# Performance work log

Hardware: AMD Instinct MI355X
Metric: run time of the kernel (lower is better)

Reference implementation:

```python
import jax, jax.numpy as jnp
import numpy as np

N = 50000   # nodes
E = 400000  # edges per relation
R = 3       # relations
IN, HID, OUT, H = 256, 64, 64, 4
NEG_SLOPE = 0.2


def setup_inputs() -> dict:
    key = jax.random.key(0)
    ks = jax.random.split(key, 16)
    w = lambda k, shape, s: jax.random.normal(k, shape, jnp.float32) * s
    sW = 1.0 / np.sqrt(IN)  # ~xavier scale (all fan-ins are 256)
    return {
        "x":   w(ks[0], (N, IN), 1.0),
        "src": jax.random.randint(ks[1], (R, E), 0, N, jnp.int32),
        "dst": jax.random.randint(ks[2], (R, E), 0, N, jnp.int32),
        "W0":  w(ks[3], (R, IN, H * HID), sW),
        "al0": w(ks[4], (R, H, HID), 0.1),
        "ar0": w(ks[5], (R, H, HID), 0.1),
        "b0":  jnp.zeros((R, H * HID), jnp.float32),
        "W1":  w(ks[6], (R, H * HID, H * HID), sW),
        "al1": w(ks[7], (R, H, HID), 0.1),
        "ar1": w(ks[8], (R, H, HID), 0.1),
        "b1":  jnp.zeros((R, H * HID), jnp.float32),
        "W2":  w(ks[9], (R, H * HID, H * OUT), sW),
        "al2": w(ks[10], (R, H, OUT), 0.1),
        "ar2": w(ks[11], (R, H, OUT), 0.1),
        "b2":  jnp.zeros((R, H * OUT), jnp.float32),
    }


def gat_conv(h, src, dst, W, al, ar, b):
    """One DGL-style GATConv with elu activation. h: (N, F_in)."""
    heads, d = al.shape
    feat = (h @ W).reshape(-1, heads, d)               # (N, H, D)
    el = jnp.einsum('nhd,hd->nh', feat, al)            # (N, H)
    er = jnp.einsum('nhd,hd->nh', feat, ar)
    e = jax.nn.leaky_relu(el[src] + er[dst], NEG_SLOPE)  # (E, H)
    # segment softmax over incoming edges of each dst node
    emax = jax.ops.segment_max(e, dst, num_segments=N)
    ex = jnp.exp(e - emax[dst])
    denom = jax.ops.segment_sum(ex, dst, num_segments=N)
    alpha = ex / jnp.maximum(denom[dst], 1e-9)         # (E, H)
    msg = feat[src] * alpha[:, :, None]                # (E, H, D)
    out = jax.ops.segment_sum(msg, dst, num_segments=N)  # (N, H, D)
    out = out + b.reshape(heads, d)
    return jax.nn.elu(out)


def _rgat(x, src, dst, params):
    h = x
    for li, (W, al, ar, b) in enumerate(params):
        outs = [gat_conv(h, src[r], dst[r], W[r], al[r], ar[r], b[r]) for r in range(R)]
        o = sum(outs) / R                              # cross-relation mean, (N, H, D)
        h = o.mean(1) if li == 2 else o.reshape(N, -1)
    return h


def reference(x, src, dst, W0, al0, ar0, b0, W1, al1, ar1, b1, W2, al2, ar2, b2):
    params = [(W0, al0, ar0, b0), (W1, al1, ar1, b1), (W2, al2, ar2, b2)]
    return _rgat(x, src, dst, params)
```

## Files before the change

### kernel.cpp

```cpp
#include <hip/hip_runtime.h>
#include <hip/hip_bf16.h>

#define N_NODES 50000
#define N_EDGES 400000
#define N_REL   3
#define NEG_SLOPE 0.2f
#define RP_STRIDE 50016
#define SCAN_BLOCKS 49
#define M_TILES 391
#define MG_PER_XCD 49
#define M_PAD 50048

typedef __bf16 bf16x8 __attribute__((ext_vector_type(8)));
typedef float  f32x4  __attribute__((ext_vector_type(4)));

static __device__ __forceinline__ float bf2f(unsigned short u) {
  return __uint_as_float(((unsigned)u) << 16);
}
static __device__ __forceinline__ unsigned short f2bf(float f) {
  union { float f; unsigned u; } x; x.f = f;
  unsigned r = x.u + 0x7FFFu + ((x.u >> 16) & 1u);
  return (unsigned short)(r >> 16);
}
static __device__ __forceinline__ void gld16(const void* g, unsigned short* lds) {
  __builtin_amdgcn_global_load_lds(
      (const __attribute__((address_space(1))) unsigned int*)g,
      (__attribute__((address_space(3))) unsigned int*)lds, 16, 0, 0);
}


__global__ void count_kernel(const int* __restrict__ dst, int* __restrict__ cnt, int total) {
  int i = blockIdx.x * 256 + threadIdx.x;
  if (i < total) {
    int r = i / N_EDGES;
    atomicAdd(&cnt[r * N_NODES + dst[i]], 1);
  }
}

__global__ void block_reduce_kernel(const int* __restrict__ cnt, int* __restrict__ psum) {
  __shared__ int s[256];
  int r = blockIdx.x / SCAN_BLOCKS, b = blockIdx.x % SCAN_BLOCKS;
  int node = b * 1024 + threadIdx.x * 4;
  int sum = 0;
  if (node + 3 < N_NODES) {
    int4 v = *(const int4*)&cnt[r * N_NODES + node];
    sum = v.x + v.y + v.z + v.w;
  } else {
    for (int j = 0; j < 4; j++)
      if (node + j < N_NODES) sum += cnt[r * N_NODES + node + j];
  }
  s[threadIdx.x] = sum;
  __syncthreads();
  for (int o = 128; o > 0; o >>= 1) {
    if (threadIdx.x < o) s[threadIdx.x] += s[threadIdx.x + o];
    __syncthreads();
  }
  if (threadIdx.x == 0) psum[r * SCAN_BLOCKS + b] = s[0];
}

__global__ void psum_scan_kernel(int* __restrict__ psum, int* __restrict__ row_ptr) {
  int r = blockIdx.x, t = threadIdx.x;
  int v = (t < SCAN_BLOCKS) ? psum[r * SCAN_BLOCKS + t] : 0;
  int incl = v;
#pragma unroll
  for (int o = 1; o < 64; o <<= 1) {
    int u = __shfl_up(incl, o);
    if (t >= o) incl += u;
  }
  if (t < SCAN_BLOCKS) psum[r * SCAN_BLOCKS + t] = incl - v;
  if (t == SCAN_BLOCKS - 1) row_ptr[r * RP_STRIDE + N_NODES] = incl;
}

__global__ void scan_write_kernel(const int* __restrict__ cnt, const int* __restrict__ psum,
                                  int* __restrict__ row_ptr, int* __restrict__ cursor) {
  __shared__ int s[256];
  int r = blockIdx.x / SCAN_BLOCKS, b = blockIdx.x % SCAN_BLOCKS;
  int tid = threadIdx.x;
  int node = b * 1024 + tid * 4;
  int c[4] = {0, 0, 0, 0};
  if (node + 3 < N_NODES) {
    int4 v = *(const int4*)&cnt[r * N_NODES + node];
    c[0] = v.x; c[1] = v.y; c[2] = v.z; c[3] = v.w;
  } else {
    for (int j = 0; j < 4; j++)
      if (node + j < N_NODES) c[j] = cnt[r * N_NODES + node + j];
  }
  int tsum = c[0] + c[1] + c[2] + c[3];
  s[tid] = tsum;
  __syncthreads();
  for (int o = 1; o < 256; o <<= 1) {
    int v = (tid >= o) ? s[tid - o] : 0;
    __syncthreads();
    s[tid] += v;
    __syncthreads();
  }
  int run = s[tid] - tsum + psum[r * SCAN_BLOCKS + b];
  if (node + 3 < N_NODES) {
    int4 rp = make_int4(run, run + c[0], run + c[0] + c[1], run + c[0] + c[1] + c[2]);
    *(int4*)&row_ptr[r * RP_STRIDE + node] = rp;
    *(int4*)&cursor[r * N_NODES + node] = rp;
  } else {
    for (int j = 0; j < 4; j++) {
      if (node + j < N_NODES) {
        row_ptr[r * RP_STRIDE + node + j] = run;
        cursor[r * N_NODES + node + j] = run;
      }
      run += c[j];
    }
  }
}

__global__ void scatter_kernel(const int* __restrict__ src, const int* __restrict__ dst,
                               int* __restrict__ cursor, int* __restrict__ col, int total) {
  int i = blockIdx.x * 256 + threadIdx.x;
  if (i < total) {
    int r = i / N_EDGES;
    int d = dst[i];
    int pos = atomicAdd(&cursor[r * N_NODES + d], 1);
    col[r * N_EDGES + pos] = src[i];
  }
}


__global__ void xsplit_kernel(const float* __restrict__ x, unsigned short* __restrict__ xh) {
  int i = blockIdx.x * 256 + threadIdx.x;
  int row = i >> 6;
  float4 v = make_float4(0.f, 0.f, 0.f, 0.f);
  if (row < N_NODES) v = ((const float4*)x)[i];
  ushort4 h;
  h.x = f2bf(v.x); h.y = f2bf(v.y); h.z = f2bf(v.z); h.w = f2bf(v.w);
  ((ushort4*)xh)[i] = h;
}


__global__ void wsplit_kernel(const float* __restrict__ W0, const float* __restrict__ W1,
                              const float* __restrict__ W2,
                              unsigned short* __restrict__ Whi, unsigned short* __restrict__ Wlo) {
  __shared__ float tile[32][33];
  int mat = blockIdx.x >> 6;
  int t = blockIdx.x & 63;
  int k0 = (t >> 3) * 32, n0 = (t & 7) * 32;
  const float* W = (mat < 3 ? W0 : (mat < 6 ? W1 : W2)) + (size_t)(mat % 3) * 65536;
  int row = threadIdx.x >> 3;
  int c4 = threadIdx.x & 7;
  float4 v = *(const float4*)&W[(k0 + row) * 256 + n0 + c4 * 4];
  tile[c4 * 4 + 0][row] = v.x;
  tile[c4 * 4 + 1][row] = v.y;
  tile[c4 * 4 + 2][row] = v.z;
  tile[c4 * 4 + 3][row] = v.w;
  __syncthreads();
  int nl = threadIdx.x >> 3;
  int kq = threadIdx.x & 7;
  ushort4 h, l;
  float a0 = tile[nl][kq * 4 + 0], a1 = tile[nl][kq * 4 + 1];
  float a2 = tile[nl][kq * 4 + 2], a3 = tile[nl][kq * 4 + 3];
  h.x = f2bf(a0); l.x = f2bf(a0 - bf2f(h.x));
  h.y = f2bf(a1); l.y = f2bf(a1 - bf2f(h.y));
  h.z = f2bf(a2); l.z = f2bf(a2 - bf2f(h.z));
  h.w = f2bf(a3); l.w = f2bf(a3 - bf2f(h.w));
  size_t o = (size_t)mat * 65536 + (n0 + nl) * 256 + k0 + kq * 4;
  *(ushort4*)&Whi[o] = h;
  *(ushort4*)&Wlo[o] = l;
}


#define LDS_S 32
#define LDT  136
#define PLANE 4096
#define BUFSZ (3 * PLANE)

__global__ __launch_bounds__(256, 3) void gemm_mfma_kernel(
    const unsigned short* __restrict__ Ah,
    const unsigned short* __restrict__ Bhi, const unsigned short* __restrict__ Blo,
    const float* __restrict__ alf, const float* __restrict__ arf,
    unsigned short* __restrict__ Cb, float* __restrict__ el, float* __restrict__ er, int M) {
  __shared__ __align__(16) unsigned short lds[2 * BUFSZ];

  const int wid = blockIdx.x;
  const int xcd = wid & 7, local = wid >> 3;
  const int m_t = (local / 6) * 8 + xcd;
  if (m_t >= M_TILES) return;
  const int n_t = local % 6;
  const int m0 = m_t * 128, n0 = n_t * 128;

  const int tid = threadIdx.x;
  const int wave = tid >> 6, lane = tid & 63;
  const int quad = lane >> 4, l16 = lane & 15;
  const int wr = wave & 1, wc = wave >> 1;

  f32x4 acc[4][4];
#pragma unroll
  for (int i = 0; i < 4; i++)
#pragma unroll
    for (int j = 0; j < 4; j++) acc[i][j] = (f32x4){0.f, 0.f, 0.f, 0.f};

  auto stage = [&](int kb, int b) {
    unsigned short* As = lds + b * BUFSZ;
#pragma unroll
    for (int i = 0; i < 2; i++) {
      int ch = wave * 2 + i;
      int c = ch * 64 + lane;
      int row = c >> 2, k16 = c & 3;
      int k16s = k16 ^ ((row >> 1) & 3);
      size_t gA = ((size_t)(m0 + row) * 256 + kb * 32) * 2 + (size_t)k16s * 16;
      size_t gB = ((size_t)(n0 + row) * 256 + kb * 32) * 2 + (size_t)k16s * 16;
      gld16((const char*)Ah + gA, &As[ch * 512]);
      gld16((const char*)Bhi + gB, &As[PLANE + ch * 512]);
      gld16((const char*)Blo + gB, &As[2 * PLANE + ch * 512]);
    }
  };

  stage(0, 0);
  __syncthreads();
  for (int kb = 0; kb < 8; kb++) {
    const int b = kb & 1;
    if (kb < 7) stage(kb + 1, b ^ 1);

    const unsigned short* As = lds + b * BUFSZ;
    const unsigned short* Bh = As + PLANE;
    const unsigned short* Bl = As + 2 * PLANE;
    bf16x8 ah[4], bh[4], bl[4];
#pragma unroll
    for (int t = 0; t < 4; t++) {
      int ar = wr * 64 + t * 16 + l16;
      int br = wc * 64 + t * 16 + l16;
      int ac = quad ^ ((ar >> 1) & 3);
      int bc = quad ^ ((br >> 1) & 3);
      ah[t] = *(const bf16x8*)&As[ar * LDS_S + ac * 8];
      bh[t] = *(const bf16x8*)&Bh[br * LDS_S + bc * 8];
      bl[t] = *(const bf16x8*)&Bl[br * LDS_S + bc * 8];
    }
#pragma unroll
    for (int mi = 0; mi < 4; mi++)
#pragma unroll
      for (int ni = 0; ni < 4; ni++) {
        acc[mi][ni] = __builtin_amdgcn_mfma_f32_16x16x32_bf16(ah[mi], bl[ni], acc[mi][ni], 0, 0, 0);
        acc[mi][ni] = __builtin_amdgcn_mfma_f32_16x16x32_bf16(ah[mi], bh[ni], acc[mi][ni], 0, 0, 0);
      }
    __syncthreads();
  }

  const int hw = n_t * 2 + wc;
  const int rel = hw >> 2, hh = hw & 3;
  float alw[4], arw[4];
#pragma unroll
  for (int ni = 0; ni < 4; ni++) {
    int gc = n0 + wc * 64 + ni * 16 + l16;
    alw[ni] = alf[gc]; arw[ni] = arf[gc];
  }
  float pel[4][4], per_[4][4];
#pragma unroll
  for (int mi = 0; mi < 4; mi++)
#pragma unroll
    for (int r = 0; r < 4; r++) {
      float se = 0.f, sr = 0.f;
#pragma unroll
      for (int ni = 0; ni < 4; ni++) {
        se += acc[mi][ni][r] * alw[ni];
        sr += acc[mi][ni][r] * arw[ni];
      }
      pel[mi][r] = se; per_[mi][r] = sr;
    }
#pragma unroll
  for (int off = 1; off < 16; off <<= 1)
#pragma unroll
    for (int mi = 0; mi < 4; mi++)
#pragma unroll
      for (int r = 0; r < 4; r++) {
        pel[mi][r] += __shfl_xor(pel[mi][r], off);
        per_[mi][r] += __shfl_xor(per_[mi][r], off);
      }
  if (l16 == 0) {
#pragma unroll
    for (int mi = 0; mi < 4; mi++)
#pragma unroll
      for (int r = 0; r < 4; r++) {
        int gm = m0 + wr * 64 + mi * 16 + quad * 4 + r;
        if (gm < M) {
          size_t o = ((size_t)rel * N_NODES + gm) * 4 + hh;
          el[o] = pel[mi][r];
          er[o] = per_[mi][r];
        }
      }
  }

#pragma unroll
  for (int mi = 0; mi < 4; mi++) {
    int row = wr * 64 + mi * 16 + quad * 4;
#pragma unroll
    for (int ni = 0; ni < 4; ni++) {
      int c = wc * 64 + ni * 16 + l16;
#pragma unroll
      for (int r = 0; r < 4; r++)
        lds[(row + r) * LDT + c] = f2bf(acc[mi][ni][r]);
    }
  }
  __syncthreads();
#pragma unroll
  for (int it = 0; it < 8; it++) {
    int chunk = tid + 256 * it;
    int row = chunk >> 4, c8 = (chunk & 15) * 8;
    int gm = m0 + row;
    if (gm < M)
      *(uint4*)&Cb[(size_t)gm * 768 + n0 + c8] = *(const uint4*)&lds[row * LDT + c8];
  }
}


#define CONSUME8(F, PN, R, BASE, a0, a1, a2, a3)                         \
  {                                                                      \
    _Pragma("unroll")                                                    \
    for (int j = 0; j < 8; j++) {                                        \
      float wj = __shfl(PN[R], (BASE + j) * 4 + hsel);                   \
      a0 += wj * bf2f(F[j].x);                                           \
      a1 += wj * bf2f(F[j].y);                                           \
      a2 += wj * bf2f(F[j].z);                                           \
      a3 += wj * bf2f(F[j].w);                                           \
    }                                                                    \
  }

#define ISSUE8(F, R, BASE)                                               \
  {                                                                      \
    const unsigned short* fb_ = featb + (R) * 256 + roffL;               \
    _Pragma("unroll")                                                    \
    for (int j = 0; j < 8; j++) {                                        \
      unsigned s_ = (unsigned)__builtin_amdgcn_readlane(sv[R], (BASE + j) * 4); \
      F[j] = *(const ushort4*)&fb_[(size_t)s_ * 768];                    \
    }                                                                    \
  }

#define REL_BODY(R, FCUR, FNXT, NR)                                      \
  {                                                                      \
    int deg = s1r[R] - s0r[R];                                           \
    if ((NR) >= 0) ISSUE8(FNXT, NR, 0);                                  \
    float a0 = 0.f, a1 = 0.f, a2 = 0.f, a3 = 0.f;                        \
    float4 bv = *(const float4*)&bias[(R) * 256 + roffL];                \
    if (deg <= 16) {                                                     \
      if (deg > 8) {                                                     \
        ushort4 g[8];                                                    \
        ISSUE8(g, R, 8);                                                 \
        CONSUME8(FCUR, pnorm, R, 0, a0, a1, a2, a3);                     \
        CONSUME8(g, pnorm, R, 8, a0, a1, a2, a3);                        \
      } else {                                                           \
        CONSUME8(FCUR, pnorm, R, 0, a0, a1, a2, a3);                     \
      }                                                                  \
    } else {                                                             \
      float ernh2 = er[((size_t)(R) * N_NODES + n) * 4 + hsel];          \
      const int* cp = col + (size_t)(R) * N_EDGES;                       \
      const unsigned short* fb_ = featb + (R) * 256 + roffL;             \
      a0 = a1 = a2 = a3 = 0.f;                                           \
      for (int i = s0r[R]; i < s1r[R]; i++) {                            \
        int s_ = cp[i];                                                  \
        float elh = el[((size_t)(R) * N_NODES + s_) * 4 + hsel];         \
        float e_ = elh + ernh2; e_ = e_ > 0.f ? e_ : NEG_SLOPE * e_;     \
        float pw = __expf(e_);                                           \
        ushort4 fA = *(const ushort4*)&fb_[(size_t)s_ * 768];            \
        a0 += pw * bf2f(fA.x); a1 += pw * bf2f(fA.y);                    \
        a2 += pw * bf2f(fA.z); a3 += pw * bf2f(fA.w);                    \
      }                                                                  \
      float inv = invsel_[R];                                            \
      a0 *= inv; a1 *= inv; a2 *= inv; a3 *= inv;                        \
    }                                                                    \
    float o0 = a0 + bv.x, o1 = a1 + bv.y, o2 = a2 + bv.z, o3 = a3 + bv.w;\
    o0 = o0 > 0.f ? o0 : __expf(o0) - 1.0f;                              \
    o1 = o1 > 0.f ? o1 : __expf(o1) - 1.0f;                              \
    o2 = o2 > 0.f ? o2 : __expf(o2) - 1.0f;                              \
    o3 = o3 > 0.f ? o3 : __expf(o3) - 1.0f;                              \
    os0 += o0 * third; os1 += o1 * third;                                \
    os2 += o2 * third; os3 += o3 * third;                                \
  }

__global__ void agg_kernel(const unsigned short* __restrict__ featb,
                           const float* __restrict__ el, const float* __restrict__ er,
                           const int* __restrict__ row_ptr, const int* __restrict__ col,
                           const float* __restrict__ bias,
                           unsigned short* __restrict__ hH, float* __restrict__ outF,
                           int final_layer) {
  int w = threadIdx.x >> 6;
  int n = blockIdx.x * 4 + w;
  int L = threadIdx.x & 63;
  if (n >= N_NODES) return;
  const int hsel = L >> 4;
  const int e1 = L >> 2, h1 = L & 3;
  const int roffL = 4 * L;

  int s0r[N_REL], s1r[N_REL], sv[N_REL];
  bool val[N_REL];
#pragma unroll
  for (int r = 0; r < N_REL; r++) {
    int s0 = row_ptr[r * RP_STRIDE + n], s1 = row_ptr[r * RP_STRIDE + n + 1];
    s0r[r] = s0; s1r[r] = s1;
    int deg = s1 - s0;
    val[r] = (e1 < deg);
    sv[r] = val[r] ? col[(size_t)r * N_EDGES + s0 + e1] : 0;
  }
  float ernh1[N_REL], elv[N_REL];
#pragma unroll
  for (int r = 0; r < N_REL; r++)
    ernh1[r] = er[((size_t)r * N_NODES + n) * 4 + h1];
#pragma unroll
  for (int r = 0; r < N_REL; r++)
    elv[r] = val[r] ? el[((size_t)r * N_NODES + sv[r]) * 4 + h1] : 0.f;

  ushort4 FA[8], FB[8];
  ISSUE8(FA, 0, 0);

  float pnorm[N_REL], invsel_[N_REL];
#pragma unroll
  for (int r = 0; r < N_REL; r++) {
    int deg = s1r[r] - s0r[r];
    float e = elv[r] + ernh1[r];
    e = e > 0.f ? e : NEG_SLOPE * e;
    float p = val[r] ? __expf(e) : 0.f;
    float d = p;
    for (int base = 16; base < deg; base += 16) {
      int e2 = base + e1;
      bool v2 = e2 < deg;
      int s = v2 ? col[(size_t)r * N_EDGES + s0r[r] + e2] : 0;
      float elx = v2 ? el[((size_t)r * N_NODES + s) * 4 + h1] : 0.f;
      float ee = elx + ernh1[r];
      ee = ee > 0.f ? ee : NEG_SLOPE * ee;
      d += v2 ? __expf(ee) : 0.f;
    }
#pragma unroll
    for (int o = 4; o < 64; o <<= 1) d += __shfl_xor(d, o);
    float rinv = 1.0f / fmaxf(d, 1e-30f);
    pnorm[r] = p * rinv;
    invsel_[r] = __shfl(rinv, hsel);
  }

  const float third = 1.0f / 3.0f;
  float os0 = 0.f, os1 = 0.f, os2 = 0.f, os3 = 0.f;
  REL_BODY(0, FA, FB, 1);
  REL_BODY(1, FB, FA, 2);
  REL_BODY(2, FA, FB, -1);

  if (final_layer) {
#pragma unroll
    for (int o = 16; o <= 32; o <<= 1) {
      os0 += __shfl_xor(os0, o); os1 += __shfl_xor(os1, o);
      os2 += __shfl_xor(os2, o); os3 += __shfl_xor(os3, o);
    }
    if (L < 16)
      *(float4*)&outF[(size_t)n * 64 + L * 4] =
          make_float4(0.25f * os0, 0.25f * os1, 0.25f * os2, 0.25f * os3);
  } else {
    ushort4 h;
    h.x = f2bf(os0); h.y = f2bf(os1); h.z = f2bf(os2); h.w = f2bf(os3);
    *(ushort4*)&hH[(size_t)n * 256 + 4 * L] = h;
  }
}


extern "C" void kernel_launch(void* const* d_in, const int* in_sizes, int n_in,
                              void* d_out, int out_size, void* d_ws, size_t ws_size,
                              hipStream_t stream) {
  (void)in_sizes; (void)n_in; (void)out_size; (void)ws_size;
  const float* x = (const float*)d_in[0];
  const int* src = (const int*)d_in[1];
  const int* dst = (const int*)d_in[2];
  const float* Wl[3]  = {(const float*)d_in[3], (const float*)d_in[7], (const float*)d_in[11]};
  const float* alL[3] = {(const float*)d_in[4], (const float*)d_in[8], (const float*)d_in[12]};
  const float* arL[3] = {(const float*)d_in[5], (const float*)d_in[9], (const float*)d_in[13]};
  const float* bL[3]  = {(const float*)d_in[6], (const float*)d_in[10], (const float*)d_in[14]};

  char* p = (char*)d_ws;
  auto alloc = [&](size_t bytes) {
    char* q = p;
    p += (bytes + 255) & ~size_t(255);
    return q;
  };
  unsigned short* xh = (unsigned short*)alloc((size_t)M_PAD * 256 * 2);
  unsigned short* hH = (unsigned short*)alloc((size_t)M_PAD * 256 * 2);
  unsigned short* featb = (unsigned short*)alloc((size_t)N_NODES * 768 * 2);
  float* el      = (float*)alloc((size_t)N_REL * N_NODES * 4 * 4);
  float* er      = (float*)alloc((size_t)N_REL * N_NODES * 4 * 4);
  int*   cnt     = (int*)alloc((size_t)N_REL * N_NODES * 4);
  int*   cursor  = (int*)alloc((size_t)N_REL * N_NODES * 4);
  int*   row_ptr = (int*)alloc((size_t)N_REL * RP_STRIDE * 4 + 64);
  int*   col     = (int*)alloc((size_t)N_REL * N_EDGES * 4);
  int*   psum    = (int*)alloc((size_t)N_REL * SCAN_BLOCKS * 4);
  unsigned short* Whi = (unsigned short*)alloc((size_t)9 * 65536 * 2);
  unsigned short* Wlo = (unsigned short*)alloc((size_t)9 * 65536 * 2);

  hipMemsetAsync(cnt, 0, (size_t)N_REL * N_NODES * 4, stream);
  const int totalE = N_REL * N_EDGES;
  count_kernel<<<(totalE + 255) / 256, 256, 0, stream>>>(dst, cnt, totalE);
  block_reduce_kernel<<<N_REL * SCAN_BLOCKS, 256, 0, stream>>>(cnt, psum);
  psum_scan_kernel<<<N_REL, 64, 0, stream>>>(psum, row_ptr);
  scan_write_kernel<<<N_REL * SCAN_BLOCKS, 256, 0, stream>>>(cnt, psum, row_ptr, cursor);
  scatter_kernel<<<(totalE + 255) / 256, 256, 0, stream>>>(src, dst, cursor, col, totalE);
  wsplit_kernel<<<9 * 64, 256, 0, stream>>>(Wl[0], Wl[1], Wl[2], Whi, Wlo);
  xsplit_kernel<<<M_PAD * 64 / 256, 256, 0, stream>>>(x, xh);

  const int nodeBlocks = (N_NODES + 3) / 4;
  const int gemmBlocks = MG_PER_XCD * 6 * 8;
  for (int l = 0; l < 3; l++) {
    const unsigned short* Ahp = (l == 0) ? xh : hH;
    gemm_mfma_kernel<<<gemmBlocks, 256, 0, stream>>>(
        Ahp, Whi + (size_t)l * 3 * 65536, Wlo + (size_t)l * 3 * 65536,
        alL[l], arL[l], featb, el, er, N_NODES);
    agg_kernel<<<nodeBlocks, 256, 0, stream>>>(
        featb, el, er, row_ptr, col, bL[l], hH, (float*)d_out, l == 2);
  }
}
```

Measured before the change: 740.6 us.

## Replace CSR build with fixed-capacity per-node buckets plus spill list

The count, block-reduce, scan and scatter kernels that built a CSR adjacency are replaced by a single fill kernel. It atomically appends each edge's source into a 16-slot bucket per (relation, destination) and sends overflow edges to a per-relation spill list. The aggregation kernel reads the degree from the counter and the neighbours from the bucket. For rare high-degree nodes it linearly scans the whole spill list for matching entries. This removes several launches and passes over the edge list, at the cost of a larger sparse bucket array and an O(spill) scan per overflowing node.

Measured after the change: 742.9 us. About the same (+0.3%).

```diff
diff --git a/kernel.cpp b/kernel.cpp
--- a/kernel.cpp
+++ b/kernel.cpp
@@ -5,11 +5,10 @@
 #define N_EDGES 400000
 #define N_REL   3
 #define NEG_SLOPE 0.2f
-#define RP_STRIDE 50016
-#define SCAN_BLOCKS 49
 #define M_TILES 391
 #define MG_PER_XCD 49
 #define M_PAD 50048
+#define ROWCAP 16
 
 typedef __bf16 bf16x8 __attribute__((ext_vector_type(8)));
 typedef float  f32x4  __attribute__((ext_vector_type(4)));
@@ -29,95 +28,19 @@
 }
 
 
-__global__ void count_kernel(const int* __restrict__ dst, int* __restrict__ cnt, int total) {
+__global__ void fill_kernel(const int* __restrict__ src, const int* __restrict__ dst,
+                            int* __restrict__ cnt, int* __restrict__ scnt,
+                            int* __restrict__ col2, int2* __restrict__ spill, int total) {
   int i = blockIdx.x * 256 + threadIdx.x;
-  if (i < total) {
-    int r = i / N_EDGES;
-    atomicAdd(&cnt[r * N_NODES + dst[i]], 1);
-  }
-}
-
-__global__ void block_reduce_kernel(const int* __restrict__ cnt, int* __restrict__ psum) {
-  __shared__ int s[256];
-  int r = blockIdx.x / SCAN_BLOCKS, b = blockIdx.x % SCAN_BLOCKS;
-  int node = b * 1024 + threadIdx.x * 4;
-  int sum = 0;
-  if (node + 3 < N_NODES) {
-    int4 v = *(const int4*)&cnt[r * N_NODES + node];
-    sum = v.x + v.y + v.z + v.w;
+  if (i >= total) return;
+  int r = i / N_EDGES;
+  int d = dst[i], s = src[i];
+  int pos = atomicAdd(&cnt[r * N_NODES + d], 1);
+  if (pos < ROWCAP) {
+    col2[((size_t)r * N_NODES + d) * ROWCAP + pos] = s;
   } else {
-    for (int j = 0; j < 4; j++)
-      if (node + j < N_NODES) sum += cnt[r * N_NODES + node + j];
-  }
-  s[threadIdx.x] = sum;
-  __syncthreads();
-  for (int o = 128; o > 0; o >>= 1) {
-    if (threadIdx.x < o) s[threadIdx.x] += s[threadIdx.x + o];
-    __syncthreads();
-  }
-  if (threadIdx.x == 0) psum[r * SCAN_BLOCKS + b] = s[0];
-}
-
-__global__ void psum_scan_kernel(int* __restrict__ psum, int* __restrict__ row_ptr) {
-  int r = blockIdx.x, t = threadIdx.x;
-  int v = (t < SCAN_BLOCKS) ? psum[r * SCAN_BLOCKS + t] : 0;
-  int incl = v;
-#pragma unroll
-  for (int o = 1; o < 64; o <<= 1) {
-    int u = __shfl_up(incl, o);
-    if (t >= o) incl += u;
-  }
-  if (t < SCAN_BLOCKS) psum[r * SCAN_BLOCKS + t] = incl - v;
-  if (t == SCAN_BLOCKS - 1) row_ptr[r * RP_STRIDE + N_NODES] = incl;
-}
-
-__global__ void scan_write_kernel(const int* __restrict__ cnt, const int* __restrict__ psum,
-                                  int* __restrict__ row_ptr, int* __restrict__ cursor) {
-  __shared__ int s[256];
-  int r = blockIdx.x / SCAN_BLOCKS, b = blockIdx.x % SCAN_BLOCKS;
-  int tid = threadIdx.x;
-  int node = b * 1024 + tid * 4;
-  int c[4] = {0, 0, 0, 0};
-  if (node + 3 < N_NODES) {
-    int4 v = *(const int4*)&cnt[r * N_NODES + node];
-    c[0] = v.x; c[1] = v.y; c[2] = v.z; c[3] = v.w;
-  } else {
-    for (int j = 0; j < 4; j++)
-      if (node + j < N_NODES) c[j] = cnt[r * N_NODES + node + j];
-  }
-  int tsum = c[0] + c[1] + c[2] + c[3];
-  s[tid] = tsum;
-  __syncthreads();
-  for (int o = 1; o < 256; o <<= 1) {
-    int v = (tid >= o) ? s[tid - o] : 0;
-    __syncthreads();
-    s[tid] += v;
-    __syncthreads();
-  }
-  int run = s[tid] - tsum + psum[r * SCAN_BLOCKS + b];
-  if (node + 3 < N_NODES) {
-    int4 rp = make_int4(run, run + c[0], run + c[0] + c[1], run + c[0] + c[1] + c[2]);
-    *(int4*)&row_ptr[r * RP_STRIDE + node] = rp;
-    *(int4*)&cursor[r * N_NODES + node] = rp;
-  } else {
-    for (int j = 0; j < 4; j++) {
-      if (node + j < N_NODES) {
-        row_ptr[r * RP_STRIDE + node + j] = run;
-        cursor[r * N_NODES + node + j] = run;
-      }
-      run += c[j];
-    }
-  }
-}
-
-__global__ void scatter_kernel(const int* __restrict__ src, const int* __restrict__ dst,
-                               int* __restrict__ cursor, int* __restrict__ col, int total) {
-  int i = blockIdx.x * 256 + threadIdx.x;
-  if (i < total) {
-    int r = i / N_EDGES;
-    int d = dst[i];
-    int pos = atomicAdd(&cursor[r * N_NODES + d], 1);
-    col[r * N_EDGES + pos] = src[i];
+    int sp = atomicAdd(&scnt[r], 1);
+    spill[(size_t)r * N_EDGES + sp] = make_int2(d, s);
   }
 }
 
@@ -331,11 +254,11 @@
 
 #define REL_BODY(R, FCUR, FNXT, NR)                                      \
   {                                                                      \
-    int deg = s1r[R] - s0r[R];                                           \
+    int deg = degr[R];                                                   \
     if ((NR) >= 0) ISSUE8(FNXT, NR, 0);                                  \
     float a0 = 0.f, a1 = 0.f, a2 = 0.f, a3 = 0.f;                        \
     float4 bv = *(const float4*)&bias[(R) * 256 + roffL];                \
-    if (deg <= 16) {                                                     \
+    if (deg <= ROWCAP) {                                                 \
       if (deg > 8) {                                                     \
         ushort4 g[8];                                                    \
         ISSUE8(g, R, 8);                                                 \
@@ -346,17 +269,30 @@
       }                                                                  \
     } else {                                                             \
       float ernh2 = er[((size_t)(R) * N_NODES + n) * 4 + hsel];          \
-      const int* cp = col + (size_t)(R) * N_EDGES;                       \
+      const int* c2 = col2 + ((size_t)(R) * N_NODES + n) * ROWCAP;       \
       const unsigned short* fb_ = featb + (R) * 256 + roffL;             \
-      a0 = a1 = a2 = a3 = 0.f;                                           \
-      for (int i = s0r[R]; i < s1r[R]; i++) {                            \
-        int s_ = cp[i];                                                  \
+      for (int j = 0; j < ROWCAP; j++) {                                 \
+        int s_ = c2[j];                                                  \
         float elh = el[((size_t)(R) * N_NODES + s_) * 4 + hsel];         \
         float e_ = elh + ernh2; e_ = e_ > 0.f ? e_ : NEG_SLOPE * e_;     \
         float pw = __expf(e_);                                           \
         ushort4 fA = *(const ushort4*)&fb_[(size_t)s_ * 768];            \
         a0 += pw * bf2f(fA.x); a1 += pw * bf2f(fA.y);                    \
         a2 += pw * bf2f(fA.z); a3 += pw * bf2f(fA.w);                    \
+      }                                                                  \
+      int sc = scnt[R];                                                  \
+      const int2* sp_ = spill + (size_t)(R) * N_EDGES;                   \
+      for (int k = 0; k < sc; k++) {                                     \
+        int2 en = sp_[k];                                                \
+        if (en.x == n) {                                                 \
+          int s_ = en.y;                                                 \
+          float elh = el[((size_t)(R) * N_NODES + s_) * 4 + hsel];       \
+          float e_ = elh + ernh2; e_ = e_ > 0.f ? e_ : NEG_SLOPE * e_;   \
+          float pw = __expf(e_);                                         \
+          ushort4 fA = *(const ushort4*)&fb_[(size_t)s_ * 768];          \
+          a0 += pw * bf2f(fA.x); a1 += pw * bf2f(fA.y);                  \
+          a2 += pw * bf2f(fA.z); a3 += pw * bf2f(fA.w);                  \
+        }                                                                \
       }                                                                  \
       float inv = invsel_[R];                                            \
       a0 *= inv; a1 *= inv; a2 *= inv; a3 *= inv;                        \
@@ -372,7 +308,8 @@
 
 __global__ void agg_kernel(const unsigned short* __restrict__ featb,
                            const float* __restrict__ el, const float* __restrict__ er,
-                           const int* __restrict__ row_ptr, const int* __restrict__ col,
+                           const int* __restrict__ cnt, const int* __restrict__ scnt,
+                           const int* __restrict__ col2, const int2* __restrict__ spill,
                            const float* __restrict__ bias,
                            unsigned short* __restrict__ hH, float* __restrict__ outF,
                            int final_layer) {
@@ -384,15 +321,15 @@
   const int e1 = L >> 2, h1 = L & 3;
   const int roffL = 4 * L;
 
-  int s0r[N_REL], s1r[N_REL], sv[N_REL];
+  int degr[N_REL], sv[N_REL];
   bool val[N_REL];
 #pragma unroll
   for (int r = 0; r < N_REL; r++) {
-    int s0 = row_ptr[r * RP_STRIDE + n], s1 = row_ptr[r * RP_STRIDE + n + 1];
-    s0r[r] = s0; s1r[r] = s1;
-    int deg = s1 - s0;
-    val[r] = (e1 < deg);
-    sv[r] = val[r] ? col[(size_t)r * N_EDGES + s0 + e1] : 0;
+    int deg = cnt[r * N_NODES + n];
+    degr[r] = deg;
+    int m16 = deg < ROWCAP ? deg : ROWCAP;
+    val[r] = (e1 < m16);
+    sv[r] = val[r] ? col2[((size_t)r * N_NODES + n) * ROWCAP + e1] : 0;
   }
   float ernh1[N_REL], elv[N_REL];
 #pragma unroll
@@ -408,19 +345,22 @@
   float pnorm[N_REL], invsel_[N_REL];
 #pragma unroll
   for (int r = 0; r < N_REL; r++) {
-    int deg = s1r[r] - s0r[r];
     float e = elv[r] + ernh1[r];
     e = e > 0.f ? e : NEG_SLOPE * e;
     float p = val[r] ? __expf(e) : 0.f;
     float d = p;
-    for (int base = 16; base < deg; base += 16) {
-      int e2 = base + e1;
-      bool v2 = e2 < deg;
-      int s = v2 ? col[(size_t)r * N_EDGES + s0r[r] + e2] : 0;
-      float elx = v2 ? el[((size_t)r * N_NODES + s) * 4 + h1] : 0.f;
-      float ee = elx + ernh1[r];
-      ee = ee > 0.f ? ee : NEG_SLOPE * ee;
-      d += v2 ? __expf(ee) : 0.f;
+    if (degr[r] > ROWCAP) {
+      int sc = scnt[r];
+      const int2* sp_ = spill + (size_t)r * N_EDGES;
+      for (int k = e1; k < sc; k += 16) {
+        int2 en = sp_[k];
+        if (en.x == n) {
+          float elx = el[((size_t)r * N_NODES + en.y) * 4 + h1];
+          float ee = elx + ernh1[r];
+          ee = ee > 0.f ? ee : NEG_SLOPE * ee;
+          d += __expf(ee);
+        }
+      }
     }
 #pragma unroll
     for (int o = 4; o < 64; o <<= 1) d += __shfl_xor(d, o);
@@ -475,21 +415,16 @@
   unsigned short* featb = (unsigned short*)alloc((size_t)N_NODES * 768 * 2);
   float* el      = (float*)alloc((size_t)N_REL * N_NODES * 4 * 4);
   float* er      = (float*)alloc((size_t)N_REL * N_NODES * 4 * 4);
-  int*   cnt     = (int*)alloc((size_t)N_REL * N_NODES * 4);
-  int*   cursor  = (int*)alloc((size_t)N_REL * N_NODES * 4);
-  int*   row_ptr = (int*)alloc((size_t)N_REL * RP_STRIDE * 4 + 64);
-  int*   col     = (int*)alloc((size_t)N_REL * N_EDGES * 4);
-  int*   psum    = (int*)alloc((size_t)N_REL * SCAN_BLOCKS * 4);
+  int*   cnt     = (int*)alloc((size_t)(N_REL * N_NODES + 16) * 4);
+  int*   col2    = (int*)alloc((size_t)N_REL * N_NODES * ROWCAP * 4);
+  int2*  spill   = (int2*)alloc((size_t)N_REL * N_EDGES * 8);
   unsigned short* Whi = (unsigned short*)alloc((size_t)9 * 65536 * 2);
   unsigned short* Wlo = (unsigned short*)alloc((size_t)9 * 65536 * 2);
-
-  hipMemsetAsync(cnt, 0, (size_t)N_REL * N_NODES * 4, stream);
+  int* scnt = cnt + N_REL * N_NODES;
+
+  hipMemsetAsync(cnt, 0, (size_t)(N_REL * N_NODES + 16) * 4, stream);
   const int totalE = N_REL * N_EDGES;
-  count_kernel<<<(totalE + 255) / 256, 256, 0, stream>>>(dst, cnt, totalE);
-  block_reduce_kernel<<<N_REL * SCAN_BLOCKS, 256, 0, stream>>>(cnt, psum);
-  psum_scan_kernel<<<N_REL, 64, 0, stream>>>(psum, row_ptr);
-  scan_write_kernel<<<N_REL * SCAN_BLOCKS, 256, 0, stream>>>(cnt, psum, row_ptr, cursor);
-  scatter_kernel<<<(totalE + 255) / 256, 256, 0, stream>>>(src, dst, cursor, col, totalE);
+  fill_kernel<<<(totalE + 255) / 256, 256, 0, stream>>>(src, dst, cnt, scnt, col2, spill, totalE);
   wsplit_kernel<<<9 * 64, 256, 0, stream>>>(Wl[0], Wl[1], Wl[2], Whi, Wlo);
   xsplit_kernel<<<M_PAD * 64 / 256, 256, 0, stream>>>(x, xh);
 
@@ -501,6 +436,6 @@
         Ahp, Whi + (size_t)l * 3 * 65536, Wlo + (size_t)l * 3 * 65536,
         alL[l], arL[l], featb, el, er, N_NODES);
     agg_kernel<<<nodeBlocks, 256, 0, stream>>>(
-        featb, el, er, row_ptr, col, bL[l], hH, (float*)d_out, l == 2);
-  }
-}
+        featb, el, er, cnt, scnt, col2, spill, bL[l], hH, (float*)d_out, l == 2);
+  }
+}
```
